# Optimization experiments

Hardware: AMD Instinct MI355X
Metric: run time of the kernel (lower is better)

Reference implementation:

```python
import jax, jax.numpy as jnp
import numpy as np

H = 32
W = 32
CIN = 64
GR = 4
CC = 6  # channels_count
N = 2


def build_a(h, w):
    # Faithful replication of the torch buffer construction (incl. overlapping
    # writes into channel 0, which accumulate multiple -1 entries per row).
    num = h * w
    a = np.zeros((num, CC, num), np.float32)
    for i in range(num):
        if (i + 1) % w != 0 and i + 1 < num:
            a[i, 0, i] = 1.0
            a[i, 0, i + 1] = -1.0
        if i + w < num:
            a[i, 1, i] = 1.0
            a[i, 1, i + w] = -1.0
        if (i + 2) % w != 0 and (i + 1) % w != 0 and (i + 2 < num):
            a[i, 2, i] = 1.0
            a[i, 2, i + 2] = -1.0
        if i + 2 * w < num:
            a[i, 3, i] = 1.0
            a[i, 3, i + 2 * w] = -1.0
        if i % w != 0 and i + w < num:
            a[i, 0, i] = 1.0
            a[i, 0, i + w - 1] = -1.0
        if (i + 1) % w != 0 and i + w < num:
            a[i, 0, i] = 1.0
            a[i, 0, i + w + 1] = -1.0
    for k in range(CC):
        a[-1, k, -1] = 1.0
    return jnp.asarray(a)


def conv2d(x, w, b, pad):
    y = jax.lax.conv_general_dilated(
        x, w, window_strides=(1, 1), padding=[(pad, pad), (pad, pad)],
        dimension_numbers=('NCHW', 'OIHW', 'NCHW'))
    return y + b[None, :, None, None]


def setup_inputs() -> dict:
    key = jax.random.key(0)
    ks = jax.random.split(key, 20)
    s = 0.05
    d = {
        'x': jax.random.normal(ks[0], (N, CIN, H, W), jnp.float32),
        'a': build_a(H, W),
        # grad branch: conv3x3 CIN->CIN, conv3x3 CIN->CC*GR
        'gw1': jax.random.normal(ks[1], (CIN, CIN, 3, 3), jnp.float32) * s,
        'gb1': jnp.zeros((CIN,), jnp.float32),
        'gw2': jax.random.normal(ks[2], (CC * GR, CIN, 3, 3), jnp.float32) * s,
        'gb2': jnp.zeros((CC * GR,), jnp.float32),
        # att branch (sigmoid at end)
        'aw1': jax.random.normal(ks[3], (CIN, CIN, 3, 3), jnp.float32) * s,
        'ab1': jnp.zeros((CIN,), jnp.float32),
        'aw2': jax.random.normal(ks[4], (CC * GR, CIN, 3, 3), jnp.float32) * s,
        'ab2': jnp.zeros((CC * GR,), jnp.float32),
        # SE branch: 1x1 CIN->CIN//2, 1x1 CIN//2->GR
        'sw1': jax.random.normal(ks[5], (CIN // 2, CIN, 1, 1), jnp.float32) * s,
        'sb1': jnp.zeros((CIN // 2,), jnp.float32),
        'sw2': jax.random.normal(ks[6], (GR, CIN // 2, 1, 1), jnp.float32) * s,
        'sb2': jnp.zeros((GR,), jnp.float32),
        # GroupNorm(1, GR) affine params
        'gn_g': jnp.ones((GR,), jnp.float32),
        'gn_b': jnp.zeros((GR,), jnp.float32),
        # post conv3x3 GR->128
        'pw': jax.random.normal(ks[7], (128, GR, 3, 3), jnp.float32) * s,
        'pb': jnp.zeros((128,), jnp.float32),
    }
    return d


def reference(x, a, gw1, gb1, gw2, gb2, aw1, ab1, aw2, ab2,
              sw1, sb1, sw2, sb2, gn_g, gn_b, pw, pb):
    n, c, h, w = x.shape
    hw = h * w
    lrelu = lambda t: jax.nn.leaky_relu(t, 0.01)

    att = jax.nn.sigmoid(conv2d(lrelu(conv2d(x, aw1, ab1, 1)), aw2, ab2, 1))
    grad = conv2d(lrelu(conv2d(x, gw1, gb1, 1)), gw2, gb2, 1)
    pooled = jnp.mean(x, axis=(2, 3), keepdims=True)
    se = jax.nn.sigmoid(conv2d(lrelu(conv2d(pooled, sw1, sb1, 0)), sw2, sb2, 0))  # [n,GR,1,1]

    b = n * GR
    att = att.reshape(b, CC, hw, 1).transpose(0, 2, 1, 3)   # [b, hw, CC, 1]
    grad = grad.reshape(b, CC, hw, 1).transpose(0, 2, 1, 3)  # [b, hw, CC, 1]

    A = (a[None] * att).reshape(b, hw * CC, hw)   # [b, hw*CC, hw]
    B = (grad * att).reshape(b, hw * CC)          # [b, hw*CC]

    ATA = jnp.einsum('bkm,bkn->bmn', A, A) + 1e-12 * jnp.eye(hw, dtype=x.dtype)
    ATB = jnp.einsum('bkm,bk->bm', A, B)[..., None]
    sol = jnp.linalg.solve(ATA, ATB).reshape(n, GR, h, w)

    # GroupNorm(1, GR): normalize over all (GR,h,w) per sample, per-channel affine
    mu = jnp.mean(sol, axis=(1, 2, 3), keepdims=True)
    var = jnp.var(sol, axis=(1, 2, 3), keepdims=True)
    y = (sol - mu) / jnp.sqrt(var + 1e-5)
    y = y * gn_g[None, :, None, None] + gn_b[None, :, None, None]

    y = se * y
    return conv2d(y, pw, pb, 1)
```

## Files before the change

kernel.cpp:

```cpp
#include <hip/hip_runtime.h>
#include <math.h>

#define HW 1024

__device__ __forceinline__ float lrelu(float v) { return v > 0.f ? v : 0.01f * v; }
__device__ __forceinline__ float sigmoidf(float v) { return 1.f / (1.f + expf(-v)); }

__device__ __forceinline__ float dpp_prev(float x) {
  return __int_as_float(__builtin_amdgcn_update_dpp(
      0, __float_as_int(x), 0x111, 0xF, 0xF, true));
}
__device__ __forceinline__ float dpp_next(float x) {
  return __int_as_float(__builtin_amdgcn_update_dpp(
      0, __float_as_int(x), 0x101, 0xF, 0xF, true));
}

__device__ __forceinline__ float block_reduce(float v, float* red, int tid) {
#pragma unroll
  for (int off = 32; off > 0; off >>= 1) v += __shfl_xor(v, off, 64);
  if ((tid & 63) == 0) red[tid >> 6] = v;
  __syncthreads();
  float s = red[0] + red[1] + red[2] + red[3];
  __syncthreads();
  return s;
}

template <int MODE>
__device__ __forceinline__ void conv_direct(
    const float* __restrict__ X,
    const float* __restrict__ Wb,
    float bias,
    float* __restrict__ outp,
    int rb) {
  __shared__ float4 sred[192];
  __shared__ float wl[576];
  int tid = threadIdx.x;
  int w = tid >> 6, l = tid & 63;
  int c4 = l & 7, ry = l >> 3;
  int r = rb * 8 + ry;
  int c0 = c4 * 4;
  float lmf = (c4 == 0) ? 0.f : 1.f;
  float rmf = (c4 == 7) ? 0.f : 1.f;
  if (tid < 144) ((float4*)wl)[tid] = ((const float4*)Wb)[tid];
  int rrc[3];
  float rmk[3];
#pragma unroll
  for (int dr = 0; dr < 3; ++dr) {
    int rr = r - 1 + dr;
    bool ok = (unsigned)rr < 32u;
    rrc[dr] = ok ? rr * 32 : 0;
    rmk[dr] = ok ? 1.f : 0.f;
  }
  __syncthreads();
  const float* Xw = X + w * 16 * HW;
  const float* Wp = wl + w * 144;
  float ax = 0.f, ay = 0.f, az = 0.f, aq = 0.f;
#pragma unroll 4
  for (int i = 0; i < 16; ++i) {
    const float* pl = Xw + i * HW;
    const float* wq = Wp + i * 9;
#pragma unroll
    for (int dr = 0; dr < 3; ++dr) {
      const float* rp = pl + rrc[dr];
      float4 m = *(const float4*)(rp + c0);
      float L = dpp_prev(m.w) * lmf;
      float R = dpp_next(m.x) * rmf;
      float w0 = wq[dr * 3 + 0] * rmk[dr];
      float w1 = wq[dr * 3 + 1] * rmk[dr];
      float w2 = wq[dr * 3 + 2] * rmk[dr];
      ax += w0 * L   + w1 * m.x + w2 * m.y;
      ay += w0 * m.x + w1 * m.y + w2 * m.z;
      az += w0 * m.y + w1 * m.z + w2 * m.w;
      aq += w0 * m.z + w1 * m.w + w2 * R;
    }
  }
  __syncthreads();
  if (w > 0) sred[(w - 1) * 64 + l] = make_float4(ax, ay, az, aq);
  __syncthreads();
  if (w == 0) {
    float4 p0 = sred[l], p1 = sred[64 + l], p2 = sred[128 + l];
    float o0 = ax + p0.x + p1.x + p2.x + bias;
    float o1 = ay + p0.y + p1.y + p2.y + bias;
    float o2 = az + p0.z + p1.z + p2.z + bias;
    float o3 = aq + p0.w + p1.w + p2.w + bias;
    if (MODE == 0) { o0 = lrelu(o0); o1 = lrelu(o1); o2 = lrelu(o2); o3 = lrelu(o3); }
    else if (MODE == 1) { o0 = sigmoidf(o0); o1 = sigmoidf(o1); o2 = sigmoidf(o2); o3 = sigmoidf(o3); }
    *(float4*)(outp + r * 32 + c0) = make_float4(o0, o1, o2, o3);
  }
}

__global__ __launch_bounds__(256) void conv64_pool(const float* __restrict__ x,
    const float* __restrict__ aw, const float* __restrict__ ab,
    const float* __restrict__ gw, const float* __restrict__ gb,
    float* __restrict__ t1, float* __restrict__ pooled) {
  int bx = blockIdx.x;
  if (bx < 1024) {
    int co = bx & 63, t = bx >> 6, rb = t & 3, g = t >> 2;
    int br = g >> 1, n = g & 1;
    conv_direct<0>(x + n * 64 * HW,
                   (br ? gw : aw) + co * 576,
                   (br ? gb : ab)[co],
                   t1 + (g * 64 + co) * HW, rb);
  } else {
    __shared__ float red[4];
    int p = bx - 1024;
    const float* px = x + p * HW;
    int tid = threadIdx.x;
    float s = px[tid] + px[tid + 256] + px[tid + 512] + px[tid + 768];
    s = block_reduce(s, red, tid);
    if (tid == 0) pooled[p] = s * (1.f / 1024.f);
  }
}

__global__ __launch_bounds__(256) void conv24_k(const float* __restrict__ t1,
    const float* __restrict__ aw2, const float* __restrict__ ab2,
    const float* __restrict__ gw2, const float* __restrict__ gb2,
    float* __restrict__ attb, float* __restrict__ gradb) {
  int bx = blockIdx.x;
  int co = bx % 24, t = bx / 24, rb = t & 3, g = t >> 2;
  int br = g >> 1, n = g & 1;
  const float* X = t1 + g * 64 * HW;
  const float* Wb = (br ? gw2 : aw2) + co * 576;
  float bias = (br ? gb2 : ab2)[co];
  float* outp = (br ? gradb : attb) + (n * 24 + co) * HW;
  if (br) conv_direct<2>(X, Wb, bias, outp, rb);
  else    conv_direct<1>(X, Wb, bias, outp, rb);
}

__global__ __launch_bounds__(256, 1) void cg_solve(const float* __restrict__ att,
    const float* __restrict__ grad, float* __restrict__ sol,
    int maxit, float tolrel) {
  int b = blockIdx.x, tid = threadIdx.x;
  __shared__ float As[7 * 1088];
  __shared__ __align__(16) float ubuf[1152];
  __shared__ float red[8];
  float* OD1  = As;
  float* OD2  = As + 1 * 1088;
  float* OD30 = As + 2 * 1088;
  float* OD31 = As + 3 * 1088;
  float* OD32 = As + 4 * 1088;
  float* OD33 = As + 5 * 1088;
  float* OD64 = As + 6 * 1088;
  for (int i = tid; i < 448; i += 256) As[(i >> 6) * 1088 + (i & 63)] = 0.f;
  if (tid < 64) { ubuf[tid] = 0.f; ubuf[1088 + tid] = 0.f; }

  const float* attb = att + b * 6 * HW;
  const float* grdb = grad + b * 6 * HW;
  const int m0 = 4 * tid;
  const int idx0 = 64 + m0;
  float rk[4], d0v[4], d0r[4];
#pragma unroll
  for (int k = 0; k < 4; ++k) {
    int m = m0 + k;
    int mr = m & 31;
    bool p1 = (mr != 31) && (m < 1023);
    bool p2 = (mr != 0) && (m < 992);
    bool p3 = (mr != 31) && (m < 992);
    bool dd = p1 | p2 | p3;
    bool c1 = m < 992;
    bool c2 = (mr != 30) && (mr != 31) && (m < 1022);
    bool c3 = m < 960;
    float a0 = attb[m],            g0 = grdb[m];
    float a1 = attb[HW + m],       g1 = grdb[HW + m];
    float a2 = attb[2 * HW + m],   g2 = grdb[2 * HW + m];
    float a3 = attb[3 * HW + m],   g3 = grdb[3 * HW + m];
    float u0 = a0 * a0, t0 = u0 * g0;
    float u1 = a1 * a1, t1 = u1 * g1;
    float u2 = a2 * a2, t2 = u2 * g2;
    float u3 = a3 * a3, t3 = u3 * g3;
    float u0m1 = 0.f, t0m1 = 0.f; bool p1m1 = false, p2m1 = false, p3m1 = false;
    if (m >= 1) {
      int j = m - 1; int jr = j & 31;
      p1m1 = (jr != 31) && (j < 1023); p2m1 = (jr != 0) && (j < 992); p3m1 = (jr != 31) && (j < 992);
      float a = attb[j], g = grdb[j]; u0m1 = a * a; t0m1 = u0m1 * g;
    }
    float u0m31 = 0.f, t0m31 = 0.f; bool p2m31 = false, p3m31 = false;
    if (m >= 31) {
      int j = m - 31; int jr = j & 31;
      p2m31 = (jr != 0) && (j < 992); p3m31 = (jr != 31) && (j < 992);
      float a = attb[j], g = grdb[j]; u0m31 = a * a; t0m31 = u0m31 * g;
    }
    float u0m33 = 0.f, t0m33 = 0.f; bool p3m33 = false;
    if (m >= 33) {
      int j = m - 33; int jr = j & 31;
      p3m33 = (jr != 31) && (j < 992);
      float a = attb[j], g = grdb[j]; u0m33 = a * a; t0m33 = u0m33 * g;
    }
    float u1m32 = 0.f, t1m32 = 0.f; bool c1m32 = false;
    if (m >= 32) {
      int j = m - 32; c1m32 = (j < 992);
      float a = attb[HW + j], g = grdb[HW + j]; u1m32 = a * a; t1m32 = u1m32 * g;
    }
    float u2m2 = 0.f, t2m2 = 0.f; bool c2m2 = false;
    if (m >= 2) {
      int j = m - 2; int jr = j & 31;
      c2m2 = (jr != 30) && (jr != 31) && (j < 1022);
      float a = attb[2 * HW + j], g = grdb[2 * HW + j]; u2m2 = a * a; t2m2 = u2m2 * g;
    }
    float u3m64 = 0.f, t3m64 = 0.f; bool c3m64 = false;
    if (m >= 64) {
      int j = m - 64; c3m64 = (j < 960);
      float a = attb[3 * HW + j], g = grdb[3 * HW + j]; u3m64 = a * a; t3m64 = u3m64 * g;
    }
    float d0 = (dd ? u0 : 0.f) + (c1 ? u1 : 0.f) + (c2 ? u2 : 0.f) + (c3 ? u3 : 0.f)
             + (p1m1 ? u0m1 : 0.f) + (p2m31 ? u0m31 : 0.f) + (p3m33 ? u0m33 : 0.f)
             + (c1m32 ? u1m32 : 0.f) + (c2m2 ? u2m2 : 0.f) + (c3m64 ? u3m64 : 0.f) + 1e-12f;
    float rhs = (dd ? t0 : 0.f) + (c1 ? t1 : 0.f) + (c2 ? t2 : 0.f) + (c3 ? t3 : 0.f)
              - (p1m1 ? t0m1 : 0.f) - (p2m31 ? t0m31 : 0.f) - (p3m33 ? t0m33 : 0.f)
              - (c1m32 ? t1m32 : 0.f) - (c2m2 ? t2m2 : 0.f) - (c3m64 ? t3m64 : 0.f);
    if (m == 1023) {
      float a4 = attb[4 * HW + 1023], g4 = grdb[4 * HW + 1023];
      float a5 = attb[5 * HW + 1023], g5 = grdb[5 * HW + 1023];
      d0 += u0 + u1 + u2 + u3 + a4 * a4 + a5 * a5;
      rhs += t0 + t1 + t2 + t3 + a4 * a4 * g4 + a5 * a5 * g5;
    }
    int idx = idx0 + k;
    OD1[idx]  = p1 ? -u0 : 0.f;
    OD31[idx] = p2 ? -u0 : 0.f;
    OD33[idx] = p3 ? -u0 : 0.f;
    OD2[idx]  = (c2 ? -u2 : 0.f) + ((p2m31 && p3m31) ? u0m31 : 0.f);
    OD30[idx] = (p1m1 && p2m1) ? u0m1 : 0.f;
    OD32[idx] = (c1 ? -u1 : 0.f) + ((p1m1 && p3m1) ? u0m1 : 0.f);
    OD64[idx] = c3 ? -u3 : 0.f;
    d0v[k] = d0;
    d0r[k] = 1.f / d0;
    rk[k] = rhs;
  }
  __syncthreads();

  float c1p[4], c1m[4], c2p[4], c2m[4], c30p[4], c30m[4], c31p[4], c31m[4];
  float c32p[4], c32m[4], c33p[4], c33m[4], c64p[4], c64m[4];
#pragma unroll
  for (int k = 0; k < 4; ++k) {
    int idx = idx0 + k;
    c1p[k]  = OD1[idx];  c1m[k]  = OD1[idx - 1];
    c2p[k]  = OD2[idx];  c2m[k]  = OD2[idx - 2];
    c30p[k] = OD30[idx]; c30m[k] = OD30[idx - 30];
    c31p[k] = OD31[idx]; c31m[k] = OD31[idx - 31];
    c32p[k] = OD32[idx]; c32m[k] = OD32[idx - 32];
    c33p[k] = OD33[idx]; c33m[k] = OD33[idx - 33];
    c64p[k] = OD64[idx]; c64m[k] = OD64[idx - 64];
  }

  float xk[4] = {0.f, 0.f, 0.f, 0.f};
  float uk[4], wk[4], pk[4], sk[4];
  const float* base = ubuf + idx0;
  int wv = tid >> 6, lane = tid & 63;

#define SPMV_AND_DOTS(GAM, DLT)                                              \
  {                                                                          \
    float2 A01 = *(const float2*)(base - 2);                                 \
    float2 A67 = *(const float2*)(base + 4);                                 \
    float2 B01 = *(const float2*)(base + 30);                                \
    float4 B25 = *(const float4*)(base + 32);                                \
    float  B6  = base[36];                                                   \
    float  C0  = base[-33];                                                  \
    float4 C14 = *(const float4*)(base - 32);                                \
    float2 C56 = *(const float2*)(base - 28);                                \
    float4 Dp  = *(const float4*)(base + 64);                                \
    float4 Ep  = *(const float4*)(base - 64);                                \
    float Aa[8] = {A01.x, A01.y, uk[0], uk[1], uk[2], uk[3], A67.x, A67.y};  \
    float Ba[7] = {B01.x, B01.y, B25.x, B25.y, B25.z, B25.w, B6};            \
    float Ca[7] = {C0, C14.x, C14.y, C14.z, C14.w, C56.x, C56.y};            \
    float Da[4] = {Dp.x, Dp.y, Dp.z, Dp.w};                                  \
    float Ea[4] = {Ep.x, Ep.y, Ep.z, Ep.w};                                  \
    GAM = 0.f; DLT = 0.f;                                                    \
    _Pragma("unroll")                                                        \
    for (int k = 0; k < 4; ++k) {                                            \
      float v = d0v[k] * uk[k];                                              \
      v += c1p[k]  * Aa[3 + k] + c1m[k]  * Aa[1 + k];                        \
      v += c2p[k]  * Aa[4 + k] + c2m[k]  * Aa[k];                            \
      v += c30p[k] * Ba[k]     + c30m[k] * Ca[3 + k];                        \
      v += c31p[k] * Ba[1 + k] + c31m[k] * Ca[2 + k];                        \
      v += c32p[k] * Ba[2 + k] + c32m[k] * Ca[1 + k];                        \
      v += c33p[k] * Ba[3 + k] + c33m[k] * Ca[k];                            \
      v += c64p[k] * Da[k]     + c64m[k] * Ea[k];                            \
      wk[k] = v;                                                             \
      GAM += rk[k] * uk[k];                                                  \
      DLT += v * uk[k];                                                      \
    }                                                                        \
    _Pragma("unroll")                                                        \
    for (int off = 32; off > 0; off >>= 1) {                                 \
      GAM += __shfl_xor(GAM, off, 64);                                       \
      DLT += __shfl_xor(DLT, off, 64);                                       \
    }                                                                        \
    if (lane == 0) { red[wv] = GAM; red[4 + wv] = DLT; }                     \
    __syncthreads();                                                         \
    GAM = red[0] + red[1] + red[2] + red[3];                                 \
    DLT = red[4] + red[5] + red[6] + red[7];                                 \
  }

#pragma unroll
  for (int k = 0; k < 4; ++k) uk[k] = rk[k] * d0r[k];
  *(float4*)(ubuf + idx0) = make_float4(uk[0], uk[1], uk[2], uk[3]);
  __syncthreads();
  float gamma, delta;
  SPMV_AND_DOTS(gamma, delta);
  if (!(fabsf(delta) > 0.f)) { goto done; }
  {
    float alpha = gamma / delta;
    float stop = gamma * tolrel;
#pragma unroll
    for (int k = 0; k < 4; ++k) {
      pk[k] = uk[k]; sk[k] = wk[k];
      xk[k] += alpha * pk[k];
      rk[k] -= alpha * sk[k];
    }
    float gamma_prev = gamma, alpha_prev = alpha;
    for (int it = 1; it < maxit; ++it) {
#pragma unroll
      for (int k = 0; k < 4; ++k) uk[k] = rk[k] * d0r[k];
      *(float4*)(ubuf + idx0) = make_float4(uk[0], uk[1], uk[2], uk[3]);
      __syncthreads();
      float g, dlt;
      SPMV_AND_DOTS(g, dlt);
      float beta = g / gamma_prev;
      float denom = dlt - beta * g / alpha_prev;
      if (!(fabsf(denom) > 0.f)) break;
      float alpha = g / denom;
#pragma unroll
      for (int k = 0; k < 4; ++k) {
        pk[k] = uk[k] + beta * pk[k];
        sk[k] = wk[k] + beta * sk[k];
        xk[k] += alpha * pk[k];
        rk[k] -= alpha * sk[k];
      }
      gamma_prev = g; alpha_prev = alpha;
      if (!(g > stop)) break;
    }
  }
done:
#pragma unroll
  for (int k = 0; k < 4; ++k) sol[b * HW + m0 + k] = xk[k];
#undef SPMV_AND_DOTS
}

__global__ __launch_bounds__(256) void gnorm_postconv(
    const float* __restrict__ sol, const float* __restrict__ pooled,
    const float* __restrict__ sw1, const float* __restrict__ sb1,
    const float* __restrict__ sw2, const float* __restrict__ sb2,
    const float* __restrict__ gn_g, const float* __restrict__ gn_b,
    const float* __restrict__ pw, const float* __restrict__ pb,
    float* __restrict__ out) {
  int bx = blockIdx.x;
  int n = bx >> 7, co = bx & 127;
  int tid = threadIdx.x;
  __shared__ __align__(16) float yp[4 * 1024];
  __shared__ float wb[36];
  __shared__ float red[4];
  __shared__ float s1[32];
  __shared__ float seg[4];
  if (tid < 36) wb[tid] = pw[co * 36 + tid];
  const float4* s4 = (const float4*)(sol + n * 4096);
  float4 v4[4];
  float sum = 0.f, ssq = 0.f;
#pragma unroll
  for (int k = 0; k < 4; ++k) {
    float4 t = s4[tid + 256 * k];
    v4[k] = t;
    sum += t.x + t.y + t.z + t.w;
    ssq += t.x * t.x + t.y * t.y + t.z * t.z + t.w * t.w;
  }
  sum = block_reduce(sum, red, tid);
  ssq = block_reduce(ssq, red, tid);
  if (tid < 32) {
    float acc = sb1[tid];
    for (int ci = 0; ci < 64; ++ci) acc += sw1[tid * 64 + ci] * pooled[n * 64 + ci];
    s1[tid] = lrelu(acc);
  }
  __syncthreads();
  if (tid < 4) {
    float acc = sb2[tid];
    for (int j = 0; j < 32; ++j) acc += sw2[tid * 32 + j] * s1[j];
    seg[tid] = sigmoidf(acc);
  }
  __syncthreads();
  float mu = sum * (1.f / 4096.f);
  float var = ssq * (1.f / 4096.f) - mu * mu;
  float inv = rsqrtf(var + 1e-5f);
#pragma unroll
  for (int k = 0; k < 4; ++k) {
    int q = tid + 256 * k;
    int g = q >> 8;
    float sA = inv * gn_g[g] * seg[g];
    float sB = (gn_b[g] - mu * inv * gn_g[g]) * seg[g];
    float4 t = v4[k];
    t.x = t.x * sA + sB;
    t.y = t.y * sA + sB;
    t.z = t.z * sA + sB;
    t.w = t.w * sA + sB;
    ((float4*)yp)[q] = t;
  }
  __syncthreads();
  float bias = pb[co];
  float acc[4] = {bias, bias, bias, bias};
#pragma unroll
  for (int k = 0; k < 4; ++k) {
    int m = tid + 256 * k;
    int yy = m >> 5, xx = m & 31;
#pragma unroll
    for (int g = 0; g < 4; ++g) {
      const float* pl = yp + g * 1024;
      const float* wc = wb + g * 9;
#pragma unroll
      for (int dy = -1; dy <= 1; ++dy) {
        int y2 = yy + dy;
        if ((unsigned)y2 < 32u) {
          const float* row = pl + y2 * 32;
#pragma unroll
          for (int dx = -1; dx <= 1; ++dx) {
            int x2 = xx + dx;
            if ((unsigned)x2 < 32u) acc[k] += row[x2] * wc[(dy + 1) * 3 + dx + 1];
          }
        }
      }
    }
  }
#pragma unroll
  for (int k = 0; k < 4; ++k) out[(n * 128 + co) * HW + tid + 256 * k] = acc[k];
}

extern "C" void kernel_launch(void* const* d_in, const int* in_sizes, int n_in,
                              void* d_out, int out_size, void* d_ws, size_t ws_size,
                              hipStream_t stream) {
  const float* x   = (const float*)d_in[0];
  const float* gw1 = (const float*)d_in[2];
  const float* gb1 = (const float*)d_in[3];
  const float* gw2 = (const float*)d_in[4];
  const float* gb2 = (const float*)d_in[5];
  const float* aw1 = (const float*)d_in[6];
  const float* ab1 = (const float*)d_in[7];
  const float* aw2 = (const float*)d_in[8];
  const float* ab2 = (const float*)d_in[9];
  const float* sw1 = (const float*)d_in[10];
  const float* sb1 = (const float*)d_in[11];
  const float* sw2 = (const float*)d_in[12];
  const float* sb2 = (const float*)d_in[13];
  const float* gng = (const float*)d_in[14];
  const float* gnb = (const float*)d_in[15];
  const float* pw  = (const float*)d_in[16];
  const float* pb  = (const float*)d_in[17];
  float* out = (float*)d_out;
  float* ws = (float*)d_ws;

  float* t1     = out;
  float* attb   = ws;
  float* gradb  = ws + 49152;
  float* pooled = ws + 98304;
  float* solv   = ws + 98432;

  conv64_pool<<<1152, 256, 0, stream>>>(x, aw1, ab1, gw1, gb1, t1, pooled);
  conv24_k<<<384, 256, 0, stream>>>(t1, aw2, ab2, gw2, gb2, attb, gradb);
  cg_solve<<<8, 256, 0, stream>>>(attb, gradb, solv, 600, 1e-5f);
  gnorm_postconv<<<256, 256, 0, stream>>>(solv, pooled, sw1, sb1, sw2, sb2,
                                          gng, gnb, pw, pb, out);
}
```

Baseline: 150.9 us.

## Switch CG solver to pipelined variant with one barrier per iteration

Rewrites the Jacobi-preconditioned CG loop as a pipelined (Ghysels-Vanroose style) CG. The dot-product reductions now overlap the next sparse matrix-vector product, using double-buffered shared vectors and DPP-based wave reductions, so each iteration needs one block barrier instead of two. It also swaps divisions for hardware reciprocal approximations and lowers the iteration cap from 600 to 400. The cost is extra vector recurrences, which can be less numerically stable, and a lower cap that may stop before convergence.

```diff
diff --git a/kernel.cpp b/kernel.cpp
--- a/kernel.cpp
+++ b/kernel.cpp
@@ -14,6 +14,23 @@
   return __int_as_float(__builtin_amdgcn_update_dpp(
       0, __float_as_int(x), 0x101, 0xF, 0xF, true));
 }
+
+template <int CTRL, int RMASK>
+__device__ __forceinline__ float dpp_add(float x) {
+  return x + __int_as_float(__builtin_amdgcn_update_dpp(
+      0, __float_as_int(x), CTRL, RMASK, 0xF, true));
+}
+__device__ __forceinline__ float wave_red_bcast(float x) {
+  x = dpp_add<0x111, 0xF>(x);
+  x = dpp_add<0x112, 0xF>(x);
+  x = dpp_add<0x114, 0xF>(x);
+  x = dpp_add<0x118, 0xF>(x);
+  x = dpp_add<0x142, 0xA>(x);
+  x = dpp_add<0x143, 0xC>(x);
+  return __int_as_float(__builtin_amdgcn_readlane(__float_as_int(x), 63));
+}
+
+__device__ __forceinline__ float frcp(float x) { return __builtin_amdgcn_rcpf(x); }
 
 __device__ __forceinline__ float block_reduce(float v, float* red, int tid) {
 #pragma unroll
@@ -132,8 +149,9 @@
     int maxit, float tolrel) {
   int b = blockIdx.x, tid = threadIdx.x;
   __shared__ float As[7 * 1088];
-  __shared__ __align__(16) float ubuf[1152];
-  __shared__ float red[8];
+  __shared__ __align__(16) float ub0[1152];
+  __shared__ __align__(16) float ub1[1152];
+  __shared__ __align__(16) float2 redb[2][4];
   float* OD1  = As;
   float* OD2  = As + 1 * 1088;
   float* OD30 = As + 2 * 1088;
@@ -142,7 +160,10 @@
   float* OD33 = As + 5 * 1088;
   float* OD64 = As + 6 * 1088;
   for (int i = tid; i < 448; i += 256) As[(i >> 6) * 1088 + (i & 63)] = 0.f;
-  if (tid < 64) { ubuf[tid] = 0.f; ubuf[1088 + tid] = 0.f; }
+  if (tid < 64) {
+    ub0[tid] = 0.f; ub0[1088 + tid] = 0.f;
+    ub1[tid] = 0.f; ub1[1088 + tid] = 0.f;
+  }
 
   const float* attb = att + b * 6 * HW;
   const float* grdb = grad + b * 6 * HW;
@@ -242,32 +263,27 @@
     c64p[k] = OD64[idx]; c64m[k] = OD64[idx - 64];
   }
 
-  float xk[4] = {0.f, 0.f, 0.f, 0.f};
-  float uk[4], wk[4], pk[4], sk[4];
-  const float* base = ubuf + idx0;
-  int wv = tid >> 6, lane = tid & 63;
-
-#define SPMV_AND_DOTS(GAM, DLT)                                              \
+#define SPMV(BASE, UK, NK)                                                   \
   {                                                                          \
-    float2 A01 = *(const float2*)(base - 2);                                 \
-    float2 A67 = *(const float2*)(base + 4);                                 \
-    float2 B01 = *(const float2*)(base + 30);                                \
-    float4 B25 = *(const float4*)(base + 32);                                \
-    float  B6  = base[36];                                                   \
-    float  C0  = base[-33];                                                  \
-    float4 C14 = *(const float4*)(base - 32);                                \
-    float2 C56 = *(const float2*)(base - 28);                                \
-    float4 Dp  = *(const float4*)(base + 64);                                \
-    float4 Ep  = *(const float4*)(base - 64);                                \
-    float Aa[8] = {A01.x, A01.y, uk[0], uk[1], uk[2], uk[3], A67.x, A67.y};  \
+    const float* bp = (BASE) + idx0;                                         \
+    float2 A01 = *(const float2*)(bp - 2);                                   \
+    float2 A67 = *(const float2*)(bp + 4);                                   \
+    float2 B01 = *(const float2*)(bp + 30);                                  \
+    float4 B25 = *(const float4*)(bp + 32);                                  \
+    float  B6  = bp[36];                                                     \
+    float  C0  = bp[-33];                                                    \
+    float4 C14 = *(const float4*)(bp - 32);                                  \
+    float2 C56 = *(const float2*)(bp - 28);                                  \
+    float4 Dp  = *(const float4*)(bp + 64);                                  \
+    float4 Ep  = *(const float4*)(bp - 64);                                  \
+    float Aa[8] = {A01.x, A01.y, UK[0], UK[1], UK[2], UK[3], A67.x, A67.y};  \
     float Ba[7] = {B01.x, B01.y, B25.x, B25.y, B25.z, B25.w, B6};            \
     float Ca[7] = {C0, C14.x, C14.y, C14.z, C14.w, C56.x, C56.y};            \
     float Da[4] = {Dp.x, Dp.y, Dp.z, Dp.w};                                  \
     float Ea[4] = {Ep.x, Ep.y, Ep.z, Ep.w};                                  \
-    GAM = 0.f; DLT = 0.f;                                                    \
     _Pragma("unroll")                                                        \
     for (int k = 0; k < 4; ++k) {                                            \
-      float v = d0v[k] * uk[k];                                              \
+      float v = d0v[k] * UK[k];                                              \
       v += c1p[k]  * Aa[3 + k] + c1m[k]  * Aa[1 + k];                        \
       v += c2p[k]  * Aa[4 + k] + c2m[k]  * Aa[k];                            \
       v += c30p[k] * Ba[k]     + c30m[k] * Ca[3 + k];                        \
@@ -275,64 +291,72 @@
       v += c32p[k] * Ba[2 + k] + c32m[k] * Ca[1 + k];                        \
       v += c33p[k] * Ba[3 + k] + c33m[k] * Ca[k];                            \
       v += c64p[k] * Da[k]     + c64m[k] * Ea[k];                            \
-      wk[k] = v;                                                             \
-      GAM += rk[k] * uk[k];                                                  \
-      DLT += v * uk[k];                                                      \
+      NK[k] = v;                                                             \
     }                                                                        \
-    _Pragma("unroll")                                                        \
-    for (int off = 32; off > 0; off >>= 1) {                                 \
-      GAM += __shfl_xor(GAM, off, 64);                                       \
-      DLT += __shfl_xor(DLT, off, 64);                                       \
-    }                                                                        \
-    if (lane == 0) { red[wv] = GAM; red[4 + wv] = DLT; }                     \
-    __syncthreads();                                                         \
-    GAM = red[0] + red[1] + red[2] + red[3];                                 \
-    DLT = red[4] + red[5] + red[6] + red[7];                                 \
-  }
+  }
+
+  int lane = tid & 63, wv = tid >> 6;
+  float xk[4] = {0.f, 0.f, 0.f, 0.f};
+  float uk[4], wk[4], mk[4], nk[4];
+  float pk[4] = {0.f, 0.f, 0.f, 0.f};
+  float sk[4] = {0.f, 0.f, 0.f, 0.f};
+  float qk[4] = {0.f, 0.f, 0.f, 0.f};
+  float zk[4] = {0.f, 0.f, 0.f, 0.f};
 
 #pragma unroll
   for (int k = 0; k < 4; ++k) uk[k] = rk[k] * d0r[k];
-  *(float4*)(ubuf + idx0) = make_float4(uk[0], uk[1], uk[2], uk[3]);
-  __syncthreads();
-  float gamma, delta;
-  SPMV_AND_DOTS(gamma, delta);
-  if (!(fabsf(delta) > 0.f)) { goto done; }
-  {
-    float alpha = gamma / delta;
-    float stop = gamma * tolrel;
+  *(float4*)(ub0 + idx0) = make_float4(uk[0], uk[1], uk[2], uk[3]);
+  __syncthreads();
+  SPMV(ub0, uk, wk);
+
+  float gp = 1.f, ap_ = 1.f, stop = 0.f;
+  for (int it = 0; it < maxit; ++it) {
+    float* bw = (it & 1) ? ub0 : ub1;
+    float2* rw = redb[it & 1];
+#pragma unroll
+    for (int k = 0; k < 4; ++k) mk[k] = wk[k] * d0r[k];
+    *(float4*)(bw + idx0) = make_float4(mk[0], mk[1], mk[2], mk[3]);
+    float gpart = 0.f, dpart = 0.f;
+#pragma unroll
+    for (int k = 0; k < 4; ++k) { gpart += rk[k] * uk[k]; dpart += wk[k] * uk[k]; }
+    float gsum = wave_red_bcast(gpart);
+    float dsum = wave_red_bcast(dpart);
+    if (lane == 0) rw[wv] = make_float2(gsum, dsum);
+    __syncthreads();
+    SPMV(bw, mk, nk);
+    float4 ra = *(float4*)&rw[0];
+    float4 rb2 = *(float4*)&rw[2];
+    float gam = ra.x + ra.z + rb2.x + rb2.z;
+    float dlt = ra.y + ra.w + rb2.y + rb2.w;
+    float beta, alpha;
+    if (it == 0) {
+      stop = gam * tolrel;
+      if (!(fabsf(dlt) > 0.f)) break;
+      beta = 0.f;
+      alpha = gam * frcp(dlt);
+    } else {
+      beta = gam * frcp(gp);
+      float denom = dlt - beta * (gam * frcp(ap_));
+      if (!(fabsf(denom) > 0.f)) break;
+      alpha = gam * frcp(denom);
+    }
 #pragma unroll
     for (int k = 0; k < 4; ++k) {
-      pk[k] = uk[k]; sk[k] = wk[k];
+      zk[k] = nk[k] + beta * zk[k];
+      qk[k] = mk[k] + beta * qk[k];
+      sk[k] = wk[k] + beta * sk[k];
+      pk[k] = uk[k] + beta * pk[k];
       xk[k] += alpha * pk[k];
       rk[k] -= alpha * sk[k];
-    }
-    float gamma_prev = gamma, alpha_prev = alpha;
-    for (int it = 1; it < maxit; ++it) {
-#pragma unroll
-      for (int k = 0; k < 4; ++k) uk[k] = rk[k] * d0r[k];
-      *(float4*)(ubuf + idx0) = make_float4(uk[0], uk[1], uk[2], uk[3]);
-      __syncthreads();
-      float g, dlt;
-      SPMV_AND_DOTS(g, dlt);
-      float beta = g / gamma_prev;
-      float denom = dlt - beta * g / alpha_prev;
-      if (!(fabsf(denom) > 0.f)) break;
-      float alpha = g / denom;
-#pragma unroll
-      for (int k = 0; k < 4; ++k) {
-        pk[k] = uk[k] + beta * pk[k];
-        sk[k] = wk[k] + beta * sk[k];
-        xk[k] += alpha * pk[k];
-        rk[k] -= alpha * sk[k];
-      }
-      gamma_prev = g; alpha_prev = alpha;
-      if (!(g > stop)) break;
-    }
-  }
-done:
+      uk[k] -= alpha * qk[k];
+      wk[k] -= alpha * zk[k];
+    }
+    gp = gam; ap_ = alpha;
+    if (!(gam > stop)) break;
+  }
 #pragma unroll
   for (int k = 0; k < 4; ++k) sol[b * HW + m0 + k] = xk[k];
-#undef SPMV_AND_DOTS
+#undef SPMV
 }
 
 __global__ __launch_bounds__(256) void gnorm_postconv(
@@ -451,7 +475,7 @@
 
   conv64_pool<<<1152, 256, 0, stream>>>(x, aw1, ab1, gw1, gb1, t1, pooled);
   conv24_k<<<384, 256, 0, stream>>>(t1, aw2, ab2, gw2, gb2, attb, gradb);
-  cg_solve<<<8, 256, 0, stream>>>(attb, gradb, solv, 600, 1e-5f);
+  cg_solve<<<8, 256, 0, stream>>>(attb, gradb, solv, 400, 1e-5f);
   gnorm_postconv<<<256, 256, 0, stream>>>(solv, pooled, sw1, sb1, sw2, sb2,
                                           gng, gnb, pw, pb, out);
 }
```

Measured after the change: 149.8 us. No clear change (-0.7%).
